# Performance work log

Measured on AMD Instinct MI355X. Metric: run time of the kernel, lower is better.

Reference implementation:

```python
import jax, jax.numpy as jnp
import numpy as np

B, S, D, H = 2, 2048, 1024, 16
DH = D // H


def setup_inputs() -> dict:
    key = jax.random.key(0)
    ks = jax.random.split(key, 7)
    scale = 1.0 / np.sqrt(D)
    return {
        "query": jax.random.normal(ks[0], (B, S, D), jnp.float32),
        "key": jax.random.normal(ks[1], (B, S, D), jnp.float32),
        "value": jax.random.normal(ks[2], (B, S, D), jnp.float32),
        # causal mask, broadcast over batch and heads
        "mask": jnp.tril(jnp.ones((S, S), bool))[None, None, :, :],
        "wq": jax.random.normal(ks[3], (D, D), jnp.float32) * scale,
        "wk": jax.random.normal(ks[4], (D, D), jnp.float32) * scale,
        "wv": jax.random.normal(ks[5], (D, D), jnp.float32) * scale,
        "wo": jax.random.normal(ks[6], (D, D), jnp.float32) * scale,
    }


def reference(query, key, value, mask, wq, wk, wv, wo):
    # nn.Linear(bias=False): y = x @ W.T
    def split_heads(x):
        return x.reshape(B, -1, H, DH).transpose(0, 2, 1, 3)  # [B,H,S,DH]

    q = split_heads(query @ wq.T)
    k = split_heads(key @ wk.T)
    v = split_heads(value @ wv.T)

    scores = jnp.einsum("bhqd,bhkd->bhqk", q, k) / jnp.sqrt(jnp.float32(DH))
    scores = jnp.where(mask, scores, jnp.float32(-1e9))
    p_attn = jax.nn.softmax(scores, axis=-1)  # dropout inactive (eval / p=0)
    x = jnp.einsum("bhqk,bhkd->bhqd", p_attn, v)
    x = x.transpose(0, 2, 1, 3).reshape(B, -1, D)
    return x @ wo.T
```

## Files before the change

kernel.cpp:

```cpp
#include <hip/hip_runtime.h>
#include <hip/hip_bf16.h>


typedef __bf16 bf16x8 __attribute__((ext_vector_type(8)));
typedef float f32x4 __attribute__((ext_vector_type(4)));

#define AS1 __attribute__((address_space(1)))
#define AS3 __attribute__((address_space(3)))

__device__ __forceinline__ void load_lds16(const void* g, void* l) {
    __builtin_amdgcn_global_load_lds((const AS1 void*)g, (AS3 void*)l, 16, 0, 0);
}

__global__ __launch_bounds__(256) void cast_many(const float* __restrict__ a0,
                                                 const float* __restrict__ a1,
                                                 const float* __restrict__ a2,
                                                 const float* __restrict__ a3,
                                                 __hip_bfloat16* __restrict__ d,
                                                 size_t per, int n4) {
    const float* s = (blockIdx.y == 0) ? a0 : (blockIdx.y == 1) ? a1 : (blockIdx.y == 2) ? a2 : a3;
    d += (size_t)blockIdx.y * per;
    int i = blockIdx.x * 256 + threadIdx.x;
    if (i >= n4) return;
    float4 v = reinterpret_cast<const float4*>(s)[i];
    union { __hip_bfloat16 h[4]; short4 s4; } u;
    u.h[0] = __float2bfloat16(v.x);
    u.h[1] = __float2bfloat16(v.y);
    u.h[2] = __float2bfloat16(v.z);
    u.h[3] = __float2bfloat16(v.w);
    reinterpret_cast<short4*>(d)[i] = u.s4;
}

template <int BM, int MODE>
__global__ __launch_bounds__(256) void gemm_bt(const __hip_bfloat16* __restrict__ Ab,
                                               const __hip_bfloat16* __restrict__ Wb,
                                               float* __restrict__ Cf,
                                               __hip_bfloat16* __restrict__ Qb,
                                               __hip_bfloat16* __restrict__ Kb,
                                               __hip_bfloat16* __restrict__ Vtb) {
    constexpr int Kn = 1024, BK = 32, MW = BM / 32;
    constexpr size_t MD = (size_t)4096 * 1024;

    __shared__ __hip_bfloat16 sA[BM * BK];
    __shared__ __hip_bfloat16 sB[128 * BK];

    const int t = threadIdx.x, w = t >> 6, l = t & 63;
    const int lr = l & 15, lk = (l >> 4) * 8;
    const int mbase = blockIdx.y * BM, nbase = blockIdx.x * 128;
    const int wr = (w >> 1) * (BM / 2), wc = (w & 1) * 64;

    const __hip_bfloat16* A = Ab;
    if constexpr (MODE == 1) A = Ab + (size_t)(nbase >> 10) * MD;

    f32x4 acc[MW][4] = {};

    for (int k0 = 0; k0 < Kn; k0 += BK) {
#pragma unroll
        for (int i = 0; i < BM / 64; i++) {
            const int c = i * 256 + t;
            load_lds16(&A[(size_t)(mbase + (c >> 2)) * Kn + k0 + (c & 3) * 8],
                       &sA[(i * 256 + w * 64) * 8]);
        }
#pragma unroll
        for (int i = 0; i < 2; i++) {
            const int c = i * 256 + t;
            load_lds16(&Wb[(size_t)(nbase + (c >> 2)) * Kn + k0 + (c & 3) * 8],
                       &sB[(i * 256 + w * 64) * 8]);
        }
        __syncthreads();
        bf16x8 af[MW], bfr[4];
#pragma unroll
        for (int m = 0; m < MW; m++) af[m] = *(const bf16x8*)&sA[(wr + m * 16 + lr) * BK + lk];
#pragma unroll
        for (int n = 0; n < 4; n++) bfr[n] = *(const bf16x8*)&sB[(wc + n * 16 + lr) * BK + lk];
#pragma unroll
        for (int m = 0; m < MW; m++)
#pragma unroll
            for (int n = 0; n < 4; n++)
                acc[m][n] = __builtin_amdgcn_mfma_f32_16x16x32_bf16(af[m], bfr[n], acc[m][n], 0, 0, 0);
        __syncthreads();
    }

    const int row0 = mbase + wr + (l >> 4) * 4;
    if constexpr (MODE == 0) {
#pragma unroll
        for (int m = 0; m < MW; m++)
#pragma unroll
            for (int n = 0; n < 4; n++)
#pragma unroll
                for (int r = 0; r < 4; r++)
                    Cf[(size_t)(row0 + m * 16 + r) * 1024 + nbase + wc + n * 16 + lr] = acc[m][n][r];
    } else {
        const int region = nbase >> 10;
        const int colL = (nbase & 1023) + wc + lr;
        if (region < 2) {
            __hip_bfloat16* Ob = (region == 0) ? Qb : Kb;
            const float alpha = (region == 0) ? 0.125f : 1.0f;
#pragma unroll
            for (int m = 0; m < MW; m++)
#pragma unroll
                for (int n = 0; n < 4; n++)
#pragma unroll
                    for (int r = 0; r < 4; r++)
                        Ob[(size_t)(row0 + m * 16 + r) * 1024 + colL + n * 16] =
                            __float2bfloat16(acc[m][n][r] * alpha);
        } else {
#pragma unroll
            for (int m = 0; m < MW; m++) {
                const int s0 = row0 + m * 16;
                const int b = s0 >> 11, s = s0 & 2047;
#pragma unroll
                for (int n = 0; n < 4; n++) {
                    const int dhg = colL + n * 16;
                    const size_t idx = ((size_t)((b * 16 + (dhg >> 6)) * 64 + (dhg & 63))) * 2048 + s;
                    union { __hip_bfloat16 h[4]; short4 s4; } u;
#pragma unroll
                    for (int r = 0; r < 4; r++) u.h[r] = __float2bfloat16(acc[m][n][r]);
                    *(short4*)&Vtb[idx] = u.s4;
                }
            }
        }
    }
}

__device__ __forceinline__ bf16x8 rd8(const __hip_bfloat16* tile, int row, int colb) {
    return *(const bf16x8*)((const char*)tile + row * 128 + (colb ^ ((row & 7) << 4)));
}

__device__ __forceinline__ void stage_kv(const char* Kg, const char* Vg, void* ksb, void* vsb, int t) {
#pragma unroll
    for (int i = 0; i < 2; i++) {
        const int c = i * 256 + t, row = c >> 3;
        const int colb = ((c & 7) * 16) ^ ((row & 7) << 4);
        load_lds16(Kg + (size_t)row * 2048 + colb, (char*)ksb + (i * 256 + (t & 192)) * 16);
    }
#pragma unroll
    for (int i = 0; i < 2; i++) {
        const int c = i * 256 + t, row = c >> 3;
        const int colb = ((c & 7) * 16) ^ ((row & 7) << 4);
        load_lds16(Vg + (size_t)row * 4096 + colb, (char*)vsb + (i * 256 + (t & 192)) * 16);
    }
}

__global__ __launch_bounds__(256) void attn_causal(const __hip_bfloat16* __restrict__ Qb,
                                                   const __hip_bfloat16* __restrict__ Kb,
                                                   const __hip_bfloat16* __restrict__ Vtb,
                                                   __hip_bfloat16* __restrict__ X) {
    constexpr int S = 2048;
    const int d0 = blockIdx.x;
    const int within = d0 >> 3;
    const int bh = (d0 & 7) * 4 + (within >> 4);
    const int p = within & 15;
    const int b = bh >> 4, h = bh & 15;
    const int qtA = p, qtB = 31 - p;

    __shared__ __hip_bfloat16 Ks[2][4096];
    __shared__ __hip_bfloat16 Vs[2][4096];
    __shared__ __hip_bfloat16 Pl[4 * 1024];

    const int t = threadIdx.x, w = t >> 6, l = t & 63;
    const int lr = l & 15, lg = l >> 4, lk = lg * 8;

    const __hip_bfloat16* Qbh = Qb + (size_t)b * S * 1024 + h * 64;
    const char* Kbh = (const char*)(Kb + (size_t)b * S * 1024 + h * 64);
    const char* Vbh = (const char*)(Vtb + (size_t)bh * 64 * 2048);
    __hip_bfloat16* Xbh = X + (size_t)b * S * 1024 + h * 64;

    int qt = qtA;
    int qrow = qt * 64 + w * 16;
    bf16x8 qf[2];
#pragma unroll
    for (int kk = 0; kk < 2; kk++)
        qf[kk] = *(const bf16x8*)&Qbh[(size_t)(qrow + lr) * 1024 + kk * 32 + lk];

    f32x4 xacc[4] = {};
    float mrow[4], lrow[4];
#pragma unroll
    for (int r = 0; r < 4; r++) { mrow[r] = -1e30f; lrow[r] = 0.f; }

    stage_kv(Kbh, Vbh, &Ks[0][0], &Vs[0][0], t);

    const int total = 33;
    int kt = 0;
    for (int i = 0; i < total; ++i) {
        if (i + 1 < total) {
            const int ktn = (i + 1 <= qtA) ? i + 1 : i - qtA;
            stage_kv(Kbh + (size_t)(ktn * 64) * 2048, Vbh + (size_t)ktn * 128,
                     &Ks[(i + 1) & 1][0], &Vs[(i + 1) & 1][0], t);
            asm volatile("s_waitcnt vmcnt(4)" ::: "memory");
        } else {
            asm volatile("s_waitcnt vmcnt(0)" ::: "memory");
        }
        __builtin_amdgcn_s_barrier();

        const __hip_bfloat16* Kt = &Ks[i & 1][0];
        const __hip_bfloat16* Vt = &Vs[i & 1][0];

        f32x4 sacc[4] = {};
#pragma unroll
        for (int kk = 0; kk < 2; kk++)
#pragma unroll
            for (int n = 0; n < 4; n++)
                sacc[n] = __builtin_amdgcn_mfma_f32_16x16x32_bf16(
                    qf[kk], rd8(Kt, n * 16 + lr, kk * 64 + lg * 16), sacc[n], 0, 0, 0);

        if (kt == qt) {
#pragma unroll
            for (int n = 0; n < 4; n++)
#pragma unroll
                for (int r = 0; r < 4; r++) {
                    const int qg = qrow + lg * 4 + r;
                    const int kv = kt * 64 + n * 16 + lr;
                    if (kv > qg) sacc[n][r] = -1e30f;
                }
        }

        float pr[4][4];
#pragma unroll
        for (int r = 0; r < 4; r++) {
            float tm = fmaxf(fmaxf(sacc[0][r], sacc[1][r]), fmaxf(sacc[2][r], sacc[3][r]));
#pragma unroll
            for (int mm = 8; mm >= 1; mm >>= 1) tm = fmaxf(tm, __shfl_xor(tm, mm, 64));
            const float mn = fmaxf(mrow[r], tm);
            const float sc = __expf(mrow[r] - mn);
            mrow[r] = mn;
            float ps = 0.f;
#pragma unroll
            for (int n = 0; n < 4; n++) {
                const float pv = __expf(sacc[n][r] - mn);
                pr[n][r] = pv;
                ps += pv;
            }
#pragma unroll
            for (int mm = 8; mm >= 1; mm >>= 1) ps += __shfl_xor(ps, mm, 64);
            lrow[r] = lrow[r] * sc + ps;
#pragma unroll
            for (int dd = 0; dd < 4; dd++) xacc[dd][r] *= sc;
        }

#pragma unroll
        for (int n = 0; n < 4; n++)
#pragma unroll
            for (int r = 0; r < 4; r++) {
                const int row = lg * 4 + r;
                *(__hip_bfloat16*)((char*)Pl + w * 2048 + row * 128 +
                                   ((n * 32 + lr * 2) ^ ((row & 7) << 4))) =
                    __float2bfloat16(pr[n][r]);
            }

#pragma unroll
        for (int kk = 0; kk < 2; kk++) {
            const bf16x8 pa = *(const bf16x8*)((const char*)Pl + w * 2048 + lr * 128 +
                                               ((kk * 64 + lg * 16) ^ ((lr & 7) << 4)));
#pragma unroll
            for (int dd = 0; dd < 4; dd++)
                xacc[dd] = __builtin_amdgcn_mfma_f32_16x16x32_bf16(
                    pa, rd8(Vt, dd * 16 + lr, kk * 64 + lg * 16), xacc[dd], 0, 0, 0);
        }

        if (i == qtA) {
#pragma unroll
            for (int r = 0; r < 4; r++) {
                const float inv = 1.0f / lrow[r];
#pragma unroll
                for (int dd = 0; dd < 4; dd++)
                    Xbh[(size_t)(qrow + lg * 4 + r) * 1024 + dd * 16 + lr] =
                        __float2bfloat16(xacc[dd][r] * inv);
            }
#pragma unroll
            for (int r = 0; r < 4; r++) { mrow[r] = -1e30f; lrow[r] = 0.f; }
#pragma unroll
            for (int dd = 0; dd < 4; dd++) xacc[dd] = f32x4{0.f, 0.f, 0.f, 0.f};
            qt = qtB;
            qrow = qt * 64 + w * 16;
#pragma unroll
            for (int kk = 0; kk < 2; kk++)
                qf[kk] = *(const bf16x8*)&Qbh[(size_t)(qrow + lr) * 1024 + kk * 32 + lk];
            kt = 0;
        } else {
            kt++;
        }
        __builtin_amdgcn_s_barrier();
    }

#pragma unroll
    for (int r = 0; r < 4; r++) {
        const float inv = 1.0f / lrow[r];
#pragma unroll
        for (int dd = 0; dd < 4; dd++)
            Xbh[(size_t)(qrow + lg * 4 + r) * 1024 + dd * 16 + lr] =
                __float2bfloat16(xacc[dd][r] * inv);
    }
}

extern "C" void kernel_launch(void* const* d_in, const int* in_sizes, int n_in,
                              void* d_out, int out_size, void* d_ws, size_t ws_size,
                              hipStream_t stream) {
    const float* q_in = (const float*)d_in[0];
    const float* k_in = (const float*)d_in[1];
    const float* v_in = (const float*)d_in[2];
    const float* wq = (const float*)d_in[4];
    const float* wk = (const float*)d_in[5];
    const float* wv = (const float*)d_in[6];
    const float* wo = (const float*)d_in[7];

    const size_t MD = (size_t)4096 * 1024;
    const size_t WD = (size_t)1024 * 1024;

    __hip_bfloat16* ws = (__hip_bfloat16*)d_ws;
    __hip_bfloat16* inb = ws;
    __hip_bfloat16* wb = inb + 3 * MD;
    __hip_bfloat16* Qbuf = wb + 4 * WD;
    __hip_bfloat16* Kbuf = Qbuf + MD;
    __hip_bfloat16* Vtb = Kbuf + MD;
    __hip_bfloat16* xb = Vtb + MD;

    cast_many<<<dim3(4096, 3), 256, 0, stream>>>(q_in, k_in, v_in, q_in, inb, MD, (int)(MD / 4));
    cast_many<<<dim3(1024, 4), 256, 0, stream>>>(wq, wk, wv, wo, wb, WD, (int)(WD / 4));

    gemm_bt<128, 1><<<dim3(24, 32), 256, 0, stream>>>(inb, wb, nullptr, Qbuf, Kbuf, Vtb);

    attn_causal<<<512, 256, 0, stream>>>(Qbuf, Kbuf, Vtb, xb);

    gemm_bt<64, 0><<<dim3(8, 64), 256, 0, stream>>>(xb, wb + 3 * WD, (float*)d_out,
                                                    nullptr, nullptr, nullptr);
}
```

Baseline: 251.5 us.

## Split paired causal query tiles into separate blocks and transpose S MFMA layout

Each block now handles one query tile, longest first, instead of pairing tile p with tile 31-p, which doubles the grid to 1024 blocks and lets the scheduler balance the uneven causal work. The QK^T MFMA operands are swapped so each lane owns one query row. That cuts the row max and sum reductions to two cross-lane shuffles and lets P be written to LDS as packed 4-element stores. Launch bounds request 4 blocks per SM for more occupancy, which may constrain registers, and the per-row rescale factors now need broadcast shuffles.

```diff
diff --git a/kernel.cpp b/kernel.cpp
--- a/kernel.cpp
+++ b/kernel.cpp
@@ -142,17 +142,16 @@
     }
 }
 
-__global__ __launch_bounds__(256) void attn_causal(const __hip_bfloat16* __restrict__ Qb,
-                                                   const __hip_bfloat16* __restrict__ Kb,
-                                                   const __hip_bfloat16* __restrict__ Vtb,
-                                                   __hip_bfloat16* __restrict__ X) {
+__global__ __launch_bounds__(256, 4) void attn_causal(const __hip_bfloat16* __restrict__ Qb,
+                                                      const __hip_bfloat16* __restrict__ Kb,
+                                                      const __hip_bfloat16* __restrict__ Vtb,
+                                                      __hip_bfloat16* __restrict__ X) {
     constexpr int S = 2048;
-    const int d0 = blockIdx.x;
-    const int within = d0 >> 3;
-    const int bh = (d0 & 7) * 4 + (within >> 4);
-    const int p = within & 15;
+    const int i0 = blockIdx.x;
+    const int j = i0 >> 3;
+    const int bh = (i0 & 7) * 4 + (j & 3);
+    const int qt = 31 - (j >> 2);
     const int b = bh >> 4, h = bh & 15;
-    const int qtA = p, qtB = 31 - p;
 
     __shared__ __hip_bfloat16 Ks[2][4096];
     __shared__ __hip_bfloat16 Vs[2][4096];
@@ -166,35 +165,30 @@
     const char* Vbh = (const char*)(Vtb + (size_t)bh * 64 * 2048);
     __hip_bfloat16* Xbh = X + (size_t)b * S * 1024 + h * 64;
 
-    int qt = qtA;
-    int qrow = qt * 64 + w * 16;
+    const int qrow = qt * 64 + w * 16;
     bf16x8 qf[2];
 #pragma unroll
     for (int kk = 0; kk < 2; kk++)
         qf[kk] = *(const bf16x8*)&Qbh[(size_t)(qrow + lr) * 1024 + kk * 32 + lk];
 
     f32x4 xacc[4] = {};
-    float mrow[4], lrow[4];
-#pragma unroll
-    for (int r = 0; r < 4; r++) { mrow[r] = -1e30f; lrow[r] = 0.f; }
+    float m = -1e30f, lsum = 0.f;
 
     stage_kv(Kbh, Vbh, &Ks[0][0], &Vs[0][0], t);
 
-    const int total = 33;
-    int kt = 0;
-    for (int i = 0; i < total; ++i) {
-        if (i + 1 < total) {
-            const int ktn = (i + 1 <= qtA) ? i + 1 : i - qtA;
-            stage_kv(Kbh + (size_t)(ktn * 64) * 2048, Vbh + (size_t)ktn * 128,
-                     &Ks[(i + 1) & 1][0], &Vs[(i + 1) & 1][0], t);
+    const int total = qt + 1;
+    for (int kt = 0; kt < total; ++kt) {
+        if (kt + 1 < total) {
+            stage_kv(Kbh + (size_t)((kt + 1) * 64) * 2048, Vbh + (size_t)(kt + 1) * 128,
+                     &Ks[(kt + 1) & 1][0], &Vs[(kt + 1) & 1][0], t);
             asm volatile("s_waitcnt vmcnt(4)" ::: "memory");
         } else {
             asm volatile("s_waitcnt vmcnt(0)" ::: "memory");
         }
         __builtin_amdgcn_s_barrier();
 
-        const __hip_bfloat16* Kt = &Ks[i & 1][0];
-        const __hip_bfloat16* Vt = &Vs[i & 1][0];
+        const __hip_bfloat16* Kt = &Ks[kt & 1][0];
+        const __hip_bfloat16* Vt = &Vs[kt & 1][0];
 
         f32x4 sacc[4] = {};
 #pragma unroll
@@ -202,51 +196,56 @@
 #pragma unroll
             for (int n = 0; n < 4; n++)
                 sacc[n] = __builtin_amdgcn_mfma_f32_16x16x32_bf16(
-                    qf[kk], rd8(Kt, n * 16 + lr, kk * 64 + lg * 16), sacc[n], 0, 0, 0);
+                    rd8(Kt, n * 16 + lr, kk * 64 + lg * 16), qf[kk], sacc[n], 0, 0, 0);
 
         if (kt == qt) {
+            const int qg = qrow + lr;
 #pragma unroll
             for (int n = 0; n < 4; n++)
 #pragma unroll
-                for (int r = 0; r < 4; r++) {
-                    const int qg = qrow + lg * 4 + r;
-                    const int kv = kt * 64 + n * 16 + lr;
-                    if (kv > qg) sacc[n][r] = -1e30f;
-                }
-        }
-
-        float pr[4][4];
-#pragma unroll
-        for (int r = 0; r < 4; r++) {
-            float tm = fmaxf(fmaxf(sacc[0][r], sacc[1][r]), fmaxf(sacc[2][r], sacc[3][r]));
-#pragma unroll
-            for (int mm = 8; mm >= 1; mm >>= 1) tm = fmaxf(tm, __shfl_xor(tm, mm, 64));
-            const float mn = fmaxf(mrow[r], tm);
-            const float sc = __expf(mrow[r] - mn);
-            mrow[r] = mn;
-            float ps = 0.f;
-#pragma unroll
-            for (int n = 0; n < 4; n++) {
+                for (int r = 0; r < 4; r++)
+                    if (kt * 64 + n * 16 + lg * 4 + r > qg) sacc[n][r] = -1e30f;
+        }
+
+        float tm = -1e30f;
+#pragma unroll
+        for (int n = 0; n < 4; n++) {
+            float a = fmaxf(fmaxf(sacc[n][0], sacc[n][1]), fmaxf(sacc[n][2], sacc[n][3]));
+            tm = fmaxf(tm, a);
+        }
+        tm = fmaxf(tm, __shfl_xor(tm, 16, 64));
+        tm = fmaxf(tm, __shfl_xor(tm, 32, 64));
+        const float mn = fmaxf(m, tm);
+        const float sc = __expf(m - mn);
+        m = mn;
+        float pr[4][4], ps = 0.f;
+#pragma unroll
+        for (int n = 0; n < 4; n++)
+#pragma unroll
+            for (int r = 0; r < 4; r++) {
                 const float pv = __expf(sacc[n][r] - mn);
                 pr[n][r] = pv;
                 ps += pv;
             }
-#pragma unroll
-            for (int mm = 8; mm >= 1; mm >>= 1) ps += __shfl_xor(ps, mm, 64);
-            lrow[r] = lrow[r] * sc + ps;
-#pragma unroll
-            for (int dd = 0; dd < 4; dd++) xacc[dd][r] *= sc;
-        }
-
-#pragma unroll
-        for (int n = 0; n < 4; n++)
-#pragma unroll
-            for (int r = 0; r < 4; r++) {
-                const int row = lg * 4 + r;
-                *(__hip_bfloat16*)((char*)Pl + w * 2048 + row * 128 +
-                                   ((n * 32 + lr * 2) ^ ((row & 7) << 4))) =
-                    __float2bfloat16(pr[n][r]);
-            }
+        ps += __shfl_xor(ps, 16, 64);
+        ps += __shfl_xor(ps, 32, 64);
+        lsum = lsum * sc + ps;
+
+#pragma unroll
+        for (int r = 0; r < 4; r++) {
+            const float bsc = __shfl(sc, (lg << 2) + r, 64);
+#pragma unroll
+            for (int dd = 0; dd < 4; dd++) xacc[dd][r] *= bsc;
+        }
+
+#pragma unroll
+        for (int n = 0; n < 4; n++) {
+            union { __hip_bfloat16 hh[4]; short4 s4; } u;
+#pragma unroll
+            for (int r = 0; r < 4; r++) u.hh[r] = __float2bfloat16(pr[n][r]);
+            *(short4*)((char*)Pl + w * 2048 + lr * 128 +
+                       ((n * 32 + lg * 8) ^ ((lr & 7) << 4))) = u.s4;
+        }
 
 #pragma unroll
         for (int kk = 0; kk < 2; kk++) {
@@ -257,39 +256,17 @@
                 xacc[dd] = __builtin_amdgcn_mfma_f32_16x16x32_bf16(
                     pa, rd8(Vt, dd * 16 + lr, kk * 64 + lg * 16), xacc[dd], 0, 0, 0);
         }
-
-        if (i == qtA) {
-#pragma unroll
-            for (int r = 0; r < 4; r++) {
-                const float inv = 1.0f / lrow[r];
-#pragma unroll
-                for (int dd = 0; dd < 4; dd++)
-                    Xbh[(size_t)(qrow + lg * 4 + r) * 1024 + dd * 16 + lr] =
-                        __float2bfloat16(xacc[dd][r] * inv);
-            }
-#pragma unroll
-            for (int r = 0; r < 4; r++) { mrow[r] = -1e30f; lrow[r] = 0.f; }
-#pragma unroll
-            for (int dd = 0; dd < 4; dd++) xacc[dd] = f32x4{0.f, 0.f, 0.f, 0.f};
-            qt = qtB;
-            qrow = qt * 64 + w * 16;
-#pragma unroll
-            for (int kk = 0; kk < 2; kk++)
-                qf[kk] = *(const bf16x8*)&Qbh[(size_t)(qrow + lr) * 1024 + kk * 32 + lk];
-            kt = 0;
-        } else {
-            kt++;
-        }
         __builtin_amdgcn_s_barrier();
     }
 
+    const float inv = 1.0f / lsum;
 #pragma unroll
     for (int r = 0; r < 4; r++) {
-        const float inv = 1.0f / lrow[r];
+        const float binv = __shfl(inv, (lg << 2) + r, 64);
 #pragma unroll
         for (int dd = 0; dd < 4; dd++)
             Xbh[(size_t)(qrow + lg * 4 + r) * 1024 + dd * 16 + lr] =
-                __float2bfloat16(xacc[dd][r] * inv);
+                __float2bfloat16(xacc[dd][r] * binv);
     }
 }
 
@@ -320,7 +297,7 @@
 
     gemm_bt<128, 1><<<dim3(24, 32), 256, 0, stream>>>(inb, wb, nullptr, Qbuf, Kbuf, Vtb);
 
-    attn_causal<<<512, 256, 0, stream>>>(Qbuf, Kbuf, Vtb, xb);
+    attn_causal<<<1024, 256, 0, stream>>>(Qbuf, Kbuf, Vtb, xb);
 
     gemm_bt<64, 0><<<dim3(8, 64), 256, 0, stream>>>(xb, wb + 3 * WD, (float*)d_out,
                                                     nullptr, nullptr, nullptr);
```

Measured after the change: 223.1 us. -11.3%, faster.
